# Optimization experiments

Hardware: AMD Instinct MI355X
Metric: run time of the kernel (lower is better)

## Reference

```python
import jax, jax.numpy as jnp
import numpy as np

WINDOW_SIZE = 64  # matches module init

def setup_inputs() -> dict:
    key = jax.random.key(0)
    kq, kk, kv = jax.random.split(key, 3)
    B, S, H, D = 1, 2048, 8, 64
    return {
        "query": jax.random.normal(kq, (B, S, H, D), dtype=jnp.float32),
        "key": jax.random.normal(kk, (B, S, H, D), dtype=jnp.float32),
        "value": jax.random.normal(kv, (B, S, H, D), dtype=jnp.float32),
    }

def reference(query, key, value):
    # Sliding-window (sparse) attention, window [i-w, i+w] inclusive.
    B, S, H, D = query.shape
    w = WINDOW_SIZE
    scale = 1.0 / jnp.sqrt(jnp.float32(D))
    offs = jnp.arange(-w, w + 1)                      # [W], W = 2w+1
    idx = jnp.arange(S)[:, None] + offs[None, :]      # [S, W]
    valid = (idx >= 0) & (idx < S)                    # [S, W]
    idx_c = jnp.clip(idx, 0, S - 1)
    k_win = key[:, idx_c]                             # [B, S, W, H, D]
    v_win = value[:, idx_c]                           # [B, S, W, H, D]
    scores = jnp.einsum('bshd,bswhd->bshw', query * scale, k_win)
    scores = jnp.where(valid[None, :, None, :], scores, -jnp.inf)
    attn = jax.nn.softmax(scores, axis=-1)            # [B, S, H, W]
    out = jnp.einsum('bshw,bswhd->bshd', attn, v_win)
    return out
```

## Files before the change

### kernel.cpp

```cpp
#include <hip/hip_runtime.h>
#include <stdint.h>

#define S_LEN 2048
#define NH    8
#define TQ    32
#define NKV   160
#define SS    161
#define PP    168
#define PVT   168

typedef __attribute__((ext_vector_type(8))) short  short8;
typedef __attribute__((ext_vector_type(4))) float  floatx4;

__device__ __forceinline__ uint16_t f2b(float f) {
  uint32_t u = __float_as_uint(f);
  u += 0x7FFFu + ((u >> 16) & 1u);
  return (uint16_t)(u >> 16);
}
__device__ __forceinline__ short8 pack8(float4 a, float4 b) {
  short8 r;
  r[0] = (short)f2b(a.x); r[1] = (short)f2b(a.y);
  r[2] = (short)f2b(a.z); r[3] = (short)f2b(a.w);
  r[4] = (short)f2b(b.x); r[5] = (short)f2b(b.y);
  r[6] = (short)f2b(b.z); r[7] = (short)f2b(b.w);
  return r;
}
__device__ __forceinline__ float wave_max(float v) {
#pragma unroll
  for (int m = 32; m >= 1; m >>= 1) v = fmaxf(v, __shfl_xor(v, m, 64));
  return v;
}
__device__ __forceinline__ float wave_sum(float v) {
#pragma unroll
  for (int m = 32; m >= 1; m >>= 1) v += __shfl_xor(v, m, 64);
  return v;
}

__global__ __launch_bounds__(256, 2)
void swa_mfma(const float* __restrict__ Q, const float* __restrict__ K,
              const float* __restrict__ V, float* __restrict__ O) {
  __shared__ float    Ssc[TQ * SS];
  __shared__ uint16_t Pw [TQ * PP];
  __shared__ uint16_t Vt [64 * PVT];

  const int tile = blockIdx.x;
  const int h    = blockIdx.y;
  const int tid  = threadIdx.x;
  const int g0   = tile * TQ - 64;

#pragma unroll
  for (int it = 0; it < 10; ++it) {
    int task = tid + it * 256;
    int d    = task & 63;
    int cq   = task >> 6;
    int gb   = g0 + (cq << 2);
    float v[4];
#pragma unroll
    for (int k = 0; k < 4; ++k) {
      int g = gb + k;
      g = g < 0 ? 0 : (g > S_LEN - 1 ? S_LEN - 1 : g);
      v[k] = V[((g * NH + h) << 6) + d];
    }
    uint32_t p01 = (uint32_t)f2b(v[0]) | ((uint32_t)f2b(v[1]) << 16);
    uint32_t p23 = (uint32_t)f2b(v[2]) | ((uint32_t)f2b(v[3]) << 16);
    uint32_t* dst = (uint32_t*)&Vt[d * PVT + (cq << 2)];
    dst[0] = p01; dst[1] = p23;
  }

  const int lane = tid & 63;
  const int w    = tid >> 6;
  const int r16  = lane & 15;
  const int quad = lane >> 4;
  const int m    = w & 1;
  const int n0   = w >> 1;

  const int qrow = tile * TQ + m * 16 + r16;
  const float* qb = Q + ((qrow * NH + h) << 6) + (quad << 3);
  float4 q0 = *(const float4*)(qb);
  float4 q1 = *(const float4*)(qb + 4);
  float4 q2 = *(const float4*)(qb + 32);
  float4 q3 = *(const float4*)(qb + 36);
  const float sc = 0.125f;
  q0.x*=sc;q0.y*=sc;q0.z*=sc;q0.w*=sc;  q1.x*=sc;q1.y*=sc;q1.z*=sc;q1.w*=sc;
  q2.x*=sc;q2.y*=sc;q2.z*=sc;q2.w*=sc;  q3.x*=sc;q3.y*=sc;q3.z*=sc;q3.w*=sc;
  short8 aq0 = pack8(q0, q1);
  short8 aq1 = pack8(q2, q3);

#pragma unroll
  for (int u = 0; u < 5; ++u) {
    int nt = n0 + 2 * u;
    int g  = g0 + nt * 16 + r16;
    g = g < 0 ? 0 : (g > S_LEN - 1 ? S_LEN - 1 : g);
    const float* kb = K + ((g * NH + h) << 6) + (quad << 3);
    float4 k0 = *(const float4*)(kb);
    float4 k1 = *(const float4*)(kb + 4);
    float4 k2 = *(const float4*)(kb + 32);
    float4 k3 = *(const float4*)(kb + 36);
    short8 b0 = pack8(k0, k1);
    short8 b1 = pack8(k2, k3);
    floatx4 acc = {0.f, 0.f, 0.f, 0.f};
    acc = __builtin_amdgcn_mfma_f32_16x16x32_bf16(aq0, b0, acc, 0, 0, 0);
    acc = __builtin_amdgcn_mfma_f32_16x16x32_bf16(aq1, b1, acc, 0, 0, 0);
    int colbase = nt * 16 + r16;
    int rowbase = m * 16 + quad * 4;
#pragma unroll
    for (int rg = 0; rg < 4; ++rg)
      Ssc[(rowbase + rg) * SS + colbase] = acc[rg];
  }
  __syncthreads();

#pragma unroll
  for (int k = 0; k < 8; ++k) {
    int r  = w * 8 + k;
    int lo = r;
    int t0 = 64 - tile * TQ;  if (t0 > lo) lo = t0;
    int hi = r + 128;
    int t1 = (S_LEN - 1) - g0; if (t1 < hi) hi = t1;
    const float* Sr = &Ssc[r * SS];
    int c0 = lane, c1 = lane + 64, c2 = lane + 128;
    int c2c = c2 > 160 ? 160 : c2;
    float s0v = Sr[c0], s1v = Sr[c1], s2v = Sr[c2c];
    bool v0 = (c0 >= lo) && (c0 <= hi);
    bool v1 = (c1 >= lo) && (c1 <= hi);
    bool v2 = (c2 >= lo) && (c2 <= hi);
    float mx = wave_max(fmaxf(fmaxf(v0 ? s0v : -INFINITY, v1 ? s1v : -INFINITY),
                              v2 ? s2v : -INFINITY));
    float e0 = v0 ? __expf(s0v - mx) : 0.f;
    float e1 = v1 ? __expf(s1v - mx) : 0.f;
    float e2 = v2 ? __expf(s2v - mx) : 0.f;
    float rs = 1.0f / wave_sum(e0 + e1 + e2);
    uint16_t* Pr = &Pw[r * PP];
    Pr[c0]  = f2b(e0 * rs);
    Pr[c1]  = f2b(e1 * rs);
    Pr[c2c] = f2b(e2 * rs);
  }
  __syncthreads();

  short8 pa[5];
  const uint16_t* Prow = &Pw[(m * 16 + r16) * PP + (quad << 3)];
#pragma unroll
  for (int kq = 0; kq < 5; ++kq)
    pa[kq] = *(const short8*)(Prow + kq * 32);

#pragma unroll
  for (int t = 0; t < 2; ++t) {
    int nt = n0 + 2 * t;
    const uint16_t* Vrow = &Vt[(nt * 16 + r16) * PVT + (quad << 3)];
    floatx4 o = {0.f, 0.f, 0.f, 0.f};
#pragma unroll
    for (int kq = 0; kq < 5; ++kq) {
      short8 bv = *(const short8*)(Vrow + kq * 32);
      o = __builtin_amdgcn_mfma_f32_16x16x32_bf16(pa[kq], bv, o, 0, 0, 0);
    }
    int orow = tile * TQ + m * 16 + quad * 4;
    int d    = nt * 16 + r16;
#pragma unroll
    for (int rg = 0; rg < 4; ++rg)
      O[(((orow + rg) * NH + h) << 6) + d] = o[rg];
  }
}

extern "C" void kernel_launch(void* const* d_in, const int* in_sizes, int n_in,
                              void* d_out, int out_size, void* d_ws, size_t ws_size,
                              hipStream_t stream) {
  const float* Q = (const float*)d_in[0];
  const float* K = (const float*)d_in[1];
  const float* V = (const float*)d_in[2];
  float* O = (float*)d_out;
  dim3 grid(S_LEN / TQ, NH);
  swa_mfma<<<grid, 256, 0, stream>>>(Q, K, V, O);
}
```

Before: 77.72 us.

## Compute softmax in MFMA registers with split-key partial stats, drop score LDS buffer

Swaps the QK^T MFMA operands so each lane holds scores for one query row, then does masking, max, exp and sum in registers using only two cross-quad shuffles. This removes the fp32 score staging buffer, one barrier and the full-wave reductions. The key range is split between two wave halves (6 and 4 tiles), each with its own partial max and sum. These are merged flash-style through a small shared array, and the PV output is rescaled per half with two accumulators. This adds exp and rescale arithmetic and leaves the work between waves uneven.

```diff
diff --git a/kernel.cpp b/kernel.cpp
--- a/kernel.cpp
+++ b/kernel.cpp
@@ -4,13 +4,12 @@
 #define S_LEN 2048
 #define NH    8
 #define TQ    32
-#define NKV   160
-#define SS    161
+#define PVT   168
 #define PP    168
-#define PVT   168
 
 typedef __attribute__((ext_vector_type(8))) short  short8;
 typedef __attribute__((ext_vector_type(4))) float  floatx4;
+typedef __attribute__((ext_vector_type(2))) unsigned int uint32x2;
 
 __device__ __forceinline__ uint16_t f2b(float f) {
   uint32_t u = __float_as_uint(f);
@@ -25,23 +24,13 @@
   r[6] = (short)f2b(b.z); r[7] = (short)f2b(b.w);
   return r;
 }
-__device__ __forceinline__ float wave_max(float v) {
-#pragma unroll
-  for (int m = 32; m >= 1; m >>= 1) v = fmaxf(v, __shfl_xor(v, m, 64));
-  return v;
-}
-__device__ __forceinline__ float wave_sum(float v) {
-#pragma unroll
-  for (int m = 32; m >= 1; m >>= 1) v += __shfl_xor(v, m, 64);
-  return v;
-}
 
 __global__ __launch_bounds__(256, 2)
 void swa_mfma(const float* __restrict__ Q, const float* __restrict__ K,
               const float* __restrict__ V, float* __restrict__ O) {
-  __shared__ float    Ssc[TQ * SS];
-  __shared__ uint16_t Pw [TQ * PP];
-  __shared__ uint16_t Vt [64 * PVT];
+  __shared__ __align__(16) uint16_t Vt[64 * PVT];
+  __shared__ __align__(16) uint16_t Pw[TQ * PP];
+  __shared__ __align__(16) float    Pp[2][16][4];
 
   const int tile = blockIdx.x;
   const int h    = blockIdx.y;
@@ -71,10 +60,12 @@
   const int w    = tid >> 6;
   const int r16  = lane & 15;
   const int quad = lane >> 4;
-  const int m    = w & 1;
-  const int n0   = w >> 1;
+  const int qt   = w & 1;
+  const int half = w >> 1;
+  const int NT   = half ? 4 : 6;
+  const int kt0  = half ? 6 : 0;
 
-  const int qrow = tile * TQ + m * 16 + r16;
+  const int qrow = tile * TQ + qt * 16 + r16;
   const float* qb = Q + ((qrow * NH + h) << 6) + (quad << 3);
   float4 q0 = *(const float4*)(qb);
   float4 q1 = *(const float4*)(qb + 4);
@@ -83,80 +74,104 @@
   const float sc = 0.125f;
   q0.x*=sc;q0.y*=sc;q0.z*=sc;q0.w*=sc;  q1.x*=sc;q1.y*=sc;q1.z*=sc;q1.w*=sc;
   q2.x*=sc;q2.y*=sc;q2.z*=sc;q2.w*=sc;  q3.x*=sc;q3.y*=sc;q3.z*=sc;q3.w*=sc;
-  short8 aq0 = pack8(q0, q1);
-  short8 aq1 = pack8(q2, q3);
+  short8 bq0 = pack8(q0, q1);
+  short8 bq1 = pack8(q2, q3);
+
+  floatx4 acc[6];
+#pragma unroll
+  for (int u = 0; u < 6; ++u) acc[u] = (floatx4){0.f, 0.f, 0.f, 0.f};
 
 #pragma unroll
-  for (int u = 0; u < 5; ++u) {
-    int nt = n0 + 2 * u;
-    int g  = g0 + nt * 16 + r16;
+  for (int u = 0; u < 6; ++u) if (u < NT) {
+    int g = g0 + (kt0 + u) * 16 + r16;
     g = g < 0 ? 0 : (g > S_LEN - 1 ? S_LEN - 1 : g);
     const float* kb = K + ((g * NH + h) << 6) + (quad << 3);
     float4 k0 = *(const float4*)(kb);
     float4 k1 = *(const float4*)(kb + 4);
     float4 k2 = *(const float4*)(kb + 32);
     float4 k3 = *(const float4*)(kb + 36);
-    short8 b0 = pack8(k0, k1);
-    short8 b1 = pack8(k2, k3);
-    floatx4 acc = {0.f, 0.f, 0.f, 0.f};
-    acc = __builtin_amdgcn_mfma_f32_16x16x32_bf16(aq0, b0, acc, 0, 0, 0);
-    acc = __builtin_amdgcn_mfma_f32_16x16x32_bf16(aq1, b1, acc, 0, 0, 0);
-    int colbase = nt * 16 + r16;
-    int rowbase = m * 16 + quad * 4;
+    short8 ak0 = pack8(k0, k1);
+    short8 ak1 = pack8(k2, k3);
+    acc[u] = __builtin_amdgcn_mfma_f32_16x16x32_bf16(ak0, bq0, acc[u], 0, 0, 0);
+    acc[u] = __builtin_amdgcn_mfma_f32_16x16x32_bf16(ak1, bq1, acc[u], 0, 0, 0);
+  }
+
+  float mx = -INFINITY;
 #pragma unroll
-    for (int rg = 0; rg < 4; ++rg)
-      Ssc[(rowbase + rg) * SS + colbase] = acc[rg];
+  for (int u = 0; u < 6; ++u) if (u < NT) {
+#pragma unroll
+    for (int r = 0; r < 4; ++r) {
+      int kpos = (kt0 + u) * 16 + (quad << 2) + r;
+      int g    = g0 + kpos;
+      bool ok  = (g >= 0) && (g < S_LEN) && (g >= qrow - 64) && (g <= qrow + 64);
+      float s  = ok ? acc[u][r] : -INFINITY;
+      acc[u][r] = s;
+      mx = fmaxf(mx, s);
+    }
   }
-  __syncthreads();
+  mx = fmaxf(mx, __shfl_xor(mx, 16, 64));
+  mx = fmaxf(mx, __shfl_xor(mx, 32, 64));
+  mx = fmaxf(mx, -3.0e38f);
 
+  float sum = 0.f;
+  uint32_t* prow = (uint32_t*)&Pw[(qt * 16 + r16) * PP];
 #pragma unroll
-  for (int k = 0; k < 8; ++k) {
-    int r  = w * 8 + k;
-    int lo = r;
-    int t0 = 64 - tile * TQ;  if (t0 > lo) lo = t0;
-    int hi = r + 128;
-    int t1 = (S_LEN - 1) - g0; if (t1 < hi) hi = t1;
-    const float* Sr = &Ssc[r * SS];
-    int c0 = lane, c1 = lane + 64, c2 = lane + 128;
-    int c2c = c2 > 160 ? 160 : c2;
-    float s0v = Sr[c0], s1v = Sr[c1], s2v = Sr[c2c];
-    bool v0 = (c0 >= lo) && (c0 <= hi);
-    bool v1 = (c1 >= lo) && (c1 <= hi);
-    bool v2 = (c2 >= lo) && (c2 <= hi);
-    float mx = wave_max(fmaxf(fmaxf(v0 ? s0v : -INFINITY, v1 ? s1v : -INFINITY),
-                              v2 ? s2v : -INFINITY));
-    float e0 = v0 ? __expf(s0v - mx) : 0.f;
-    float e1 = v1 ? __expf(s1v - mx) : 0.f;
-    float e2 = v2 ? __expf(s2v - mx) : 0.f;
-    float rs = 1.0f / wave_sum(e0 + e1 + e2);
-    uint16_t* Pr = &Pw[r * PP];
-    Pr[c0]  = f2b(e0 * rs);
-    Pr[c1]  = f2b(e1 * rs);
-    Pr[c2c] = f2b(e2 * rs);
+  for (int u = 0; u < 6; ++u) if (u < NT) {
+    float e0 = __expf(acc[u][0] - mx);
+    float e1 = __expf(acc[u][1] - mx);
+    float e2 = __expf(acc[u][2] - mx);
+    float e3 = __expf(acc[u][3] - mx);
+    sum += (e0 + e1) + (e2 + e3);
+    uint32x2 pw;
+    pw[0] = (uint32_t)f2b(e0) | ((uint32_t)f2b(e1) << 16);
+    pw[1] = (uint32_t)f2b(e2) | ((uint32_t)f2b(e3) << 16);
+    int ci = (kt0 + u) * 16 + (quad << 2);
+    *(uint32x2*)&prow[ci >> 1] = pw;
   }
+  sum += __shfl_xor(sum, 16, 64);
+  sum += __shfl_xor(sum, 32, 64);
+  if (quad == 0) {
+    Pp[qt][r16][half * 2]     = mx;
+    Pp[qt][r16][half * 2 + 1] = sum;
+  }
+
   __syncthreads();
 
   short8 pa[5];
-  const uint16_t* Prow = &Pw[(m * 16 + r16) * PP + (quad << 3)];
+  const uint16_t* Pr = &Pw[(qt * 16 + r16) * PP + (quad << 3)];
 #pragma unroll
-  for (int kq = 0; kq < 5; ++kq)
-    pa[kq] = *(const short8*)(Prow + kq * 32);
+  for (int kt = 0; kt < 5; ++kt)
+    pa[kt] = *(const short8*)(Pr + kt * 32);
+
+  float ca[4], cb[4];
+#pragma unroll
+  for (int r = 0; r < 4; ++r) {
+    float4 p = *(const float4*)(&Pp[qt][(quad << 2) + r][0]);
+    float m  = fmaxf(p.x, p.z);
+    float f0 = __expf(p.x - m);
+    float f1 = __expf(p.z - m);
+    float rs = 1.0f / (f0 * p.y + f1 * p.w);
+    ca[r] = f0 * rs;
+    cb[r] = f1 * rs;
+  }
 
 #pragma unroll
   for (int t = 0; t < 2; ++t) {
-    int nt = n0 + 2 * t;
-    const uint16_t* Vrow = &Vt[(nt * 16 + r16) * PVT + (quad << 3)];
-    floatx4 o = {0.f, 0.f, 0.f, 0.f};
+    int dt = half * 2 + t;
+    const uint16_t* Vr = &Vt[(dt * 16 + r16) * PVT + (quad << 3)];
+    floatx4 oA = {0.f, 0.f, 0.f, 0.f};
+    floatx4 oB = {0.f, 0.f, 0.f, 0.f};
 #pragma unroll
-    for (int kq = 0; kq < 5; ++kq) {
-      short8 bv = *(const short8*)(Vrow + kq * 32);
-      o = __builtin_amdgcn_mfma_f32_16x16x32_bf16(pa[kq], bv, o, 0, 0, 0);
-    }
-    int orow = tile * TQ + m * 16 + quad * 4;
-    int d    = nt * 16 + r16;
+    for (int kt = 0; kt < 3; ++kt)
+      oA = __builtin_amdgcn_mfma_f32_16x16x32_bf16(pa[kt], *(const short8*)(Vr + kt * 32), oA, 0, 0, 0);
 #pragma unroll
-    for (int rg = 0; rg < 4; ++rg)
-      O[(((orow + rg) * NH + h) << 6) + d] = o[rg];
+    for (int kt = 3; kt < 5; ++kt)
+      oB = __builtin_amdgcn_mfma_f32_16x16x32_bf16(pa[kt], *(const short8*)(Vr + kt * 32), oB, 0, 0, 0);
+    int orow = tile * TQ + qt * 16 + (quad << 2);
+    int d    = dt * 16 + r16;
+#pragma unroll
+    for (int r = 0; r < 4; ++r)
+      O[(((orow + r) * NH + h) << 6) + d] = ca[r] * oA[r] + cb[r] * oB[r];
   }
 }
 
```

Result: faster. 75.54 us (-2.8%).
